# Optimization experiments

Measured on AMD Instinct MI355X. Metric: run time of the kernel, lower is better.

## Reference

```python
import jax, jax.numpy as jnp
import numpy as np


def setup_inputs() -> dict:
    key = jax.random.key(0)
    ks = jax.random.split(key, 5)
    B, S, H, F, E = 2, 2048, 768, 1536, 8
    scale_h = 1.0 / np.sqrt(H)
    scale_f = 1.0 / np.sqrt(F)
    return {
        "hidden_states": jax.random.normal(ks[0], (B, S, H), dtype=jnp.float32),
        "gate_w": jax.random.normal(ks[1], (E, H), dtype=jnp.float32) * scale_h,
        "w1": jax.random.normal(ks[2], (E, F, H), dtype=jnp.float32) * scale_h,
        "w3": jax.random.normal(ks[3], (E, F, H), dtype=jnp.float32) * scale_h,
        "w2": jax.random.normal(ks[4], (E, H, F), dtype=jnp.float32) * scale_f,
        "k": 2,
    }


def reference(hidden_states, gate_w, w1, w3, w2, k):
    B, S, H = hidden_states.shape
    E = gate_w.shape[0]
    x = hidden_states.reshape(-1, H)                     # [T, H]
    T = x.shape[0]

    # Router: softmax in fp32, top-k, renormalize among selected experts.
    router_logits = x @ gate_w.T                         # [T, E]
    probs = jax.nn.softmax(router_logits.astype(jnp.float32), axis=-1)
    top_w, top_i = jax.lax.top_k(probs, k)               # [T, k]
    top_w = top_w / jnp.sum(top_w, axis=-1, keepdims=True)
    top_w = top_w.astype(x.dtype)

    # Scatter top-k weights into dense [T, E] combine weights (0 for unselected).
    combine = jnp.zeros((T, E), dtype=x.dtype)
    combine = combine.at[jnp.arange(T)[:, None], top_i].set(top_w)

    # SwiGLU experts (zero-weight experts contribute exactly 0 to the sum).
    g = jnp.einsum("th,efh->tef", x, w1)                 # [T, E, F]
    u = jnp.einsum("th,efh->tef", x, w3)                 # [T, E, F]
    act = jax.nn.silu(g) * u                             # [T, E, F]
    expert_out = jnp.einsum("tef,ehf->teh", act, w2)     # [T, E, H]
    y = jnp.einsum("te,teh->th", combine, expert_out)    # [T, H]

    return y.reshape(B, S, H), router_logits
```

## Files before the change

kernel.cpp:

```cpp
#include <hip/hip_runtime.h>
#include <hip/hip_bf16.h>

#define T_TOK 4096
#define H_DIM 768
#define E_NUM 8
#define F_DIM 1536

typedef __bf16 bf16x8 __attribute__((ext_vector_type(8)));
typedef unsigned short u16x8 __attribute__((ext_vector_type(8)));
typedef float f32x4 __attribute__((ext_vector_type(4)));
typedef unsigned int u32;

__device__ __forceinline__ unsigned short f2bf(float f) {
    unsigned int u = __float_as_uint(f);
    u += 0x7FFF + ((u >> 16) & 1);
    return (unsigned short)(u >> 16);
}

__device__ __forceinline__ float bf2f(unsigned short s) {
    unsigned int u = ((unsigned int)s) << 16;
    return __uint_as_float(u);
}

__device__ __forceinline__ void gload16(const unsigned short* g, unsigned short* l) {
    __builtin_amdgcn_global_load_lds(
        (const __attribute__((address_space(1))) u32*)(g),
        (__attribute__((address_space(3))) u32*)(l),
        16, 0, 0);
}

__global__ __launch_bounds__(256) void router_kernel(
    const float* __restrict__ x,
    const float* __restrict__ gw,
    float* __restrict__ logits_out,
    float* __restrict__ weight,
    int* __restrict__ eidx,
    unsigned short* __restrict__ xb) {
    int t = blockIdx.x * 4 + (threadIdx.x >> 6);
    int lane = threadIdx.x & 63;

    const float4* xr = reinterpret_cast<const float4*>(x + (size_t)t * H_DIM);
    float4 xv[3];
#pragma unroll
    for (int i = 0; i < 3; ++i) xv[i] = xr[i * 64 + lane];

    unsigned short* xbr = xb + (size_t)t * H_DIM;
#pragma unroll
    for (int i = 0; i < 3; ++i) {
        ushort4 o;
        o.x = f2bf(xv[i].x); o.y = f2bf(xv[i].y);
        o.z = f2bf(xv[i].z); o.w = f2bf(xv[i].w);
        *reinterpret_cast<ushort4*>(xbr + (i * 64 + lane) * 4) = o;
    }

    float v[E_NUM];
#pragma unroll
    for (int e = 0; e < E_NUM; ++e) {
        const float4* g = reinterpret_cast<const float4*>(gw + e * H_DIM);
        float p = 0.f;
#pragma unroll
        for (int i = 0; i < 3; ++i) {
            float4 gv = g[i * 64 + lane];
            p += xv[i].x * gv.x + xv[i].y * gv.y + xv[i].z * gv.z + xv[i].w * gv.w;
        }
        v[e] = p;
    }
#pragma unroll
    for (int d = 1; d < 8; d <<= 1)
#pragma unroll
        for (int e = 0; e < E_NUM; ++e) v[e] += __shfl_xor(v[e], d);
    int me = lane & 7;
    float le = v[0];
#pragma unroll
    for (int e = 1; e < E_NUM; ++e) le = (me == e) ? v[e] : le;
#pragma unroll
    for (int d = 8; d < 64; d <<= 1) le += __shfl_xor(le, d);

    if (lane < 8) logits_out[t * E_NUM + lane] = le;

    float m0 = le;
#pragma unroll
    for (int d = 1; d < 8; d <<= 1) m0 = fmaxf(m0, __shfl_xor(m0, d));
    unsigned long long b0 = __ballot(le == m0);
    int e0 = (__ffsll((long long)b0) - 1) & 7;
    float le1 = (me == e0) ? -3.4e38f : le;
    float m1 = le1;
#pragma unroll
    for (int d = 1; d < 8; d <<= 1) m1 = fmaxf(m1, __shfl_xor(m1, d));
    unsigned long long b1 = __ballot(le1 == m1);
    int e1 = (__ffsll((long long)b1) - 1) & 7;

    if (lane == 0) {
        float w0 = 1.f / (1.f + __expf(m1 - m0));
        weight[t * 2 + 0] = w0;
        weight[t * 2 + 1] = 1.f - w0;
        eidx[t] = e0 | (e1 << 8);
    }
}

__global__ __launch_bounds__(256) void build_lists_kernel(
    const int* __restrict__ eidx,
    int* __restrict__ list,
    int* __restrict__ counts) {
    int e = blockIdx.x;
    int tid = threadIdx.x;
    int lane = tid & 63;
    int wv = tid >> 6;
    __shared__ int wsum[4];
    __shared__ int wbase[4];
    __shared__ int sbase;
    if (tid == 0) sbase = 0;
    __syncthreads();
    for (int c = 0; c < T_TOK; c += 256) {
        int tok = c + tid;
        int pk = eidx[tok];
        int slot = -1;
        if ((pk & 255) == e) slot = tok * 2;
        else if ((pk >> 8) == e) slot = tok * 2 + 1;
        unsigned long long m = __ballot(slot >= 0);
        int prefix = __popcll(m & ((1ull << lane) - 1ull));
        if (lane == 0) wsum[wv] = __popcll(m);
        __syncthreads();
        if (tid == 0) {
            int s = sbase;
#pragma unroll
            for (int i = 0; i < 4; ++i) { wbase[i] = s; s += wsum[i]; }
            sbase = s;
        }
        __syncthreads();
        if (slot >= 0) list[e * T_TOK + wbase[wv] + prefix] = slot;
        __syncthreads();
    }
    if (tid == 0) counts[e] = sbase;
}

__global__ __launch_bounds__(256, 3) void gemm13_kernel(
    const unsigned short* __restrict__ xb,
    const float* __restrict__ w1,
    const float* __restrict__ w3,
    const int* __restrict__ list,
    const int* __restrict__ counts,
    unsigned short* __restrict__ act) {
    int orig = blockIdx.x;
    int wg = (orig & 7) * 768 + (orig >> 3);
    int tm = wg & 31;
    int tn = (wg >> 5) % 24;
    int e = wg / (32 * 24);

    int cnt = counts[e];
    if (tm * 128 >= cnt) return;
    const int* lst = list + e * T_TOK + tm * 128;
    int mrem = cnt - tm * 128;

    __shared__ unsigned short sA[2][128 * 32];
    __shared__ unsigned short sB1[2][64 * 32];
    __shared__ unsigned short sB3[2][64 * 32];

    int tid = threadIdx.x;
    int lane = tid & 63;
    int wid = tid >> 6;

    int r0 = tid >> 2;
    int r1 = r0 + 64;
    int c8 = ((tid & 3) ^ ((r0 >> 1) & 3)) * 8;
    int ldsOff = r0 * 32 + (tid & 3) * 8;
    int tok0 = lst[(r0 < mrem) ? r0 : 0] >> 1;
    int tok1 = lst[(r1 < mrem) ? r1 : 0] >> 1;
    const unsigned short* gA0 = xb + (size_t)tok0 * H_DIM + c8;
    const unsigned short* gA1 = xb + (size_t)tok1 * H_DIM + c8;
    const float* gw1 = w1 + ((size_t)e * F_DIM + tn * 64 + r0) * H_DIM + c8;
    const float* gw3 = w3 + ((size_t)e * F_DIM + tn * 64 + r0) * H_DIM + c8;

    auto writeB = [&](int b, float4 x1a, float4 x1b, float4 x3a, float4 x3b) {
        u16x8 o1, o3;
        o1[0] = f2bf(x1a.x); o1[1] = f2bf(x1a.y); o1[2] = f2bf(x1a.z); o1[3] = f2bf(x1a.w);
        o1[4] = f2bf(x1b.x); o1[5] = f2bf(x1b.y); o1[6] = f2bf(x1b.z); o1[7] = f2bf(x1b.w);
        o3[0] = f2bf(x3a.x); o3[1] = f2bf(x3a.y); o3[2] = f2bf(x3a.z); o3[3] = f2bf(x3a.w);
        o3[4] = f2bf(x3b.x); o3[5] = f2bf(x3b.y); o3[6] = f2bf(x3b.z); o3[7] = f2bf(x3b.w);
        *reinterpret_cast<u16x8*>(&sB1[b][ldsOff]) = o1;
        *reinterpret_cast<u16x8*>(&sB3[b][ldsOff]) = o3;
    };

    int wr = (wid >> 1) * 64;
    int wc = (wid & 1) * 32;
    int fr = lane & 15;
    int kb = ((lane >> 4) ^ ((lane >> 1) & 3)) * 8;

    f32x4 accG[4][2] = {};
    f32x4 accU[4][2] = {};

    const int NT = H_DIM / 32;

    {
        float4 p1a = *reinterpret_cast<const float4*>(gw1);
        float4 p1b = *reinterpret_cast<const float4*>(gw1 + 4);
        float4 p3a = *reinterpret_cast<const float4*>(gw3);
        float4 p3b = *reinterpret_cast<const float4*>(gw3 + 4);
        gload16(gA0, &sA[0][wid * 512]);
        gload16(gA1, &sA[0][2048 + wid * 512]);
        writeB(0, p1a, p1b, p3a, p3b);
    }
    __syncthreads();

    int cur = 0;
    for (int t = 0; t < NT; ++t) {
        float4 n1a, n1b, n3a, n3b;
        bool pre = (t + 1 < NT);
        if (pre) {
            int kt = (t + 1) * 32;
            n1a = *reinterpret_cast<const float4*>(gw1 + kt);
            n1b = *reinterpret_cast<const float4*>(gw1 + kt + 4);
            n3a = *reinterpret_cast<const float4*>(gw3 + kt);
            n3b = *reinterpret_cast<const float4*>(gw3 + kt + 4);
            gload16(gA0 + kt, &sA[cur ^ 1][wid * 512]);
            gload16(gA1 + kt, &sA[cur ^ 1][2048 + wid * 512]);
        }

        bf16x8 a[4], b1[2], b3[2];
#pragma unroll
        for (int mi = 0; mi < 4; ++mi)
            a[mi] = *reinterpret_cast<const bf16x8*>(&sA[cur][(wr + mi * 16 + fr) * 32 + kb]);
#pragma unroll
        for (int ni = 0; ni < 2; ++ni) {
            b1[ni] = *reinterpret_cast<const bf16x8*>(&sB1[cur][(wc + ni * 16 + fr) * 32 + kb]);
            b3[ni] = *reinterpret_cast<const bf16x8*>(&sB3[cur][(wc + ni * 16 + fr) * 32 + kb]);
        }
#pragma unroll
        for (int mi = 0; mi < 4; ++mi)
#pragma unroll
            for (int ni = 0; ni < 2; ++ni) {
                accG[mi][ni] = __builtin_amdgcn_mfma_f32_16x16x32_bf16(a[mi], b1[ni], accG[mi][ni], 0, 0, 0);
                accU[mi][ni] = __builtin_amdgcn_mfma_f32_16x16x32_bf16(a[mi], b3[ni], accU[mi][ni], 0, 0, 0);
            }

        if (pre) writeB(cur ^ 1, n1a, n1b, n3a, n3b);
        __syncthreads();
        cur ^= 1;
    }

    int rg = (lane >> 4) * 4;
    int ci = lane & 15;
#pragma unroll
    for (int mi = 0; mi < 4; ++mi) {
#pragma unroll
        for (int r = 0; r < 4; ++r) {
            int m = wr + mi * 16 + rg + r;
            if (m >= mrem) continue;
            int entry = lst[m];
            size_t rowOff = (size_t)entry * F_DIM + tn * 64;
#pragma unroll
            for (int ni = 0; ni < 2; ++ni) {
                float g = accG[mi][ni][r];
                float u = accU[mi][ni][r];
                float s = g / (1.f + __expf(-g));
                act[rowOff + wc + ni * 16 + ci] = f2bf(s * u);
            }
        }
    }
}

__global__ __launch_bounds__(256, 3) void gemm2_kernel(
    const unsigned short* __restrict__ act,
    const float* __restrict__ w2,
    const int* __restrict__ list,
    const int* __restrict__ counts,
    const float* __restrict__ weight,
    unsigned short* __restrict__ ybuf) {
    int orig = blockIdx.x;
    int wg = (orig & 7) * 192 + (orig >> 3);
    int tm = wg & 31;
    int tn = (wg >> 5) % 6;
    int e = wg / (32 * 6);

    int cnt = counts[e];
    if (tm * 128 >= cnt) return;
    const int* lst = list + e * T_TOK + tm * 128;
    int mrem = cnt - tm * 128;

    __shared__ unsigned short sA[2][128 * 32];
    __shared__ unsigned short sB[2][128 * 32];

    int tid = threadIdx.x;
    int lane = tid & 63;
    int wid = tid >> 6;

    int r0 = tid >> 2;
    int r1 = r0 + 64;
    int c8 = ((tid & 3) ^ ((r0 >> 1) & 3)) * 8;
    int ldsOff = r0 * 32 + (tid & 3) * 8;
    int row0 = lst[(r0 < mrem) ? r0 : 0];
    int row1 = lst[(r1 < mrem) ? r1 : 0];
    const unsigned short* gA0 = act + (size_t)row0 * F_DIM + c8;
    const unsigned short* gA1 = act + (size_t)row1 * F_DIM + c8;
    const float* gw2a = w2 + ((size_t)e * H_DIM + tn * 128 + r0) * F_DIM + c8;
    const float* gw2b = gw2a + (size_t)64 * F_DIM;

    auto writeB = [&](int b, float4 xa0, float4 xa1, float4 xb0, float4 xb1) {
        u16x8 oa, ob;
        oa[0] = f2bf(xa0.x); oa[1] = f2bf(xa0.y); oa[2] = f2bf(xa0.z); oa[3] = f2bf(xa0.w);
        oa[4] = f2bf(xa1.x); oa[5] = f2bf(xa1.y); oa[6] = f2bf(xa1.z); oa[7] = f2bf(xa1.w);
        ob[0] = f2bf(xb0.x); ob[1] = f2bf(xb0.y); ob[2] = f2bf(xb0.z); ob[3] = f2bf(xb0.w);
        ob[4] = f2bf(xb1.x); ob[5] = f2bf(xb1.y); ob[6] = f2bf(xb1.z); ob[7] = f2bf(xb1.w);
        *reinterpret_cast<u16x8*>(&sB[b][ldsOff]) = oa;
        *reinterpret_cast<u16x8*>(&sB[b][2048 + ldsOff]) = ob;
    };

    int wr = (wid >> 1) * 64;
    int wc = (wid & 1) * 64;
    int fr = lane & 15;
    int kb = ((lane >> 4) ^ ((lane >> 1) & 3)) * 8;

    f32x4 acc[4][4] = {};

    const int NT = F_DIM / 32;

    {
        float4 pa0 = *reinterpret_cast<const float4*>(gw2a);
        float4 pa1 = *reinterpret_cast<const float4*>(gw2a + 4);
        float4 pb0 = *reinterpret_cast<const float4*>(gw2b);
        float4 pb1 = *reinterpret_cast<const float4*>(gw2b + 4);
        gload16(gA0, &sA[0][wid * 512]);
        gload16(gA1, &sA[0][2048 + wid * 512]);
        writeB(0, pa0, pa1, pb0, pb1);
    }
    __syncthreads();

    int cur = 0;
    for (int t = 0; t < NT; ++t) {
        float4 na0, na1, nb0, nb1;
        bool pre = (t + 1 < NT);
        if (pre) {
            int kt = (t + 1) * 32;
            na0 = *reinterpret_cast<const float4*>(gw2a + kt);
            na1 = *reinterpret_cast<const float4*>(gw2a + kt + 4);
            nb0 = *reinterpret_cast<const float4*>(gw2b + kt);
            nb1 = *reinterpret_cast<const float4*>(gw2b + kt + 4);
            gload16(gA0 + kt, &sA[cur ^ 1][wid * 512]);
            gload16(gA1 + kt, &sA[cur ^ 1][2048 + wid * 512]);
        }

        bf16x8 a[4], b[4];
#pragma unroll
        for (int mi = 0; mi < 4; ++mi)
            a[mi] = *reinterpret_cast<const bf16x8*>(&sA[cur][(wr + mi * 16 + fr) * 32 + kb]);
#pragma unroll
        for (int ni = 0; ni < 4; ++ni)
            b[ni] = *reinterpret_cast<const bf16x8*>(&sB[cur][(wc + ni * 16 + fr) * 32 + kb]);
#pragma unroll
        for (int mi = 0; mi < 4; ++mi)
#pragma unroll
            for (int ni = 0; ni < 4; ++ni)
                acc[mi][ni] = __builtin_amdgcn_mfma_f32_16x16x32_bf16(a[mi], b[ni], acc[mi][ni], 0, 0, 0);

        if (pre) writeB(cur ^ 1, na0, na1, nb0, nb1);
        __syncthreads();
        cur ^= 1;
    }

    int rg = (lane >> 4) * 4;
    int ci = lane & 15;
#pragma unroll
    for (int mi = 0; mi < 4; ++mi) {
#pragma unroll
        for (int r = 0; r < 4; ++r) {
            int m = wr + mi * 16 + rg + r;
            if (m >= mrem) continue;
            int entry = lst[m];
            float wv = weight[entry];
            size_t rowOff = (size_t)entry * H_DIM + tn * 128;
#pragma unroll
            for (int ni = 0; ni < 4; ++ni)
                ybuf[rowOff + wc + ni * 16 + ci] = f2bf(acc[mi][ni][r] * wv);
        }
    }
}

__global__ __launch_bounds__(256) void combine_kernel(
    const unsigned short* __restrict__ ybuf, float* __restrict__ y) {
    int v = blockIdx.x * blockDim.x + threadIdx.x;
    if (v >= T_TOK * H_DIM / 8) return;
    int t = v / (H_DIM / 8);
    int hv = (v % (H_DIM / 8)) * 8;
    const ushort4* pa = reinterpret_cast<const ushort4*>(ybuf + (size_t)(2 * t) * H_DIM + hv);
    const ushort4* pb = reinterpret_cast<const ushort4*>(ybuf + (size_t)(2 * t + 1) * H_DIM + hv);
    float* yo = y + (size_t)t * H_DIM + hv;
#pragma unroll
    for (int h = 0; h < 2; ++h) {
        ushort4 a = pa[h];
        ushort4 b = pb[h];
        float4 r;
        r.x = bf2f(a.x) + bf2f(b.x);
        r.y = bf2f(a.y) + bf2f(b.y);
        r.z = bf2f(a.z) + bf2f(b.z);
        r.w = bf2f(a.w) + bf2f(b.w);
        *reinterpret_cast<float4*>(yo + h * 4) = r;
    }
}

extern "C" void kernel_launch(void* const* d_in, const int* in_sizes, int n_in,
                              void* d_out, int out_size, void* d_ws, size_t ws_size,
                              hipStream_t stream) {
    const float* x  = (const float*)d_in[0];
    const float* gw = (const float*)d_in[1];
    const float* w1 = (const float*)d_in[2];
    const float* w3 = (const float*)d_in[3];
    const float* w2 = (const float*)d_in[4];

    float* y = (float*)d_out;
    float* logits_out = y + (size_t)T_TOK * H_DIM;

    char* ws = (char*)d_ws;
    size_t off = 0;
    auto alloc = [&](size_t bytes) -> char* {
        char* p = ws + off;
        off += (bytes + 255) & ~(size_t)255;
        return p;
    };
    unsigned short* xb   = (unsigned short*)alloc((size_t)T_TOK * H_DIM * 2);
    unsigned short* act  = (unsigned short*)alloc((size_t)T_TOK * 2 * F_DIM * 2);
    unsigned short* ybuf = (unsigned short*)alloc((size_t)T_TOK * 2 * H_DIM * 2);
    float* weight = (float*)alloc((size_t)T_TOK * 2 * 4);
    int* list     = (int*)alloc((size_t)E_NUM * T_TOK * 4);
    int* counts   = (int*)alloc((size_t)E_NUM * 4);
    int* eidx     = (int*)alloc((size_t)T_TOK * 4);

    router_kernel<<<T_TOK / 4, 256, 0, stream>>>(x, gw, logits_out, weight, eidx, xb);

    build_lists_kernel<<<E_NUM, 256, 0, stream>>>(eidx, list, counts);

    gemm13_kernel<<<6144, 256, 0, stream>>>(xb, w1, w3, list, counts, act);

    gemm2_kernel<<<1536, 256, 0, stream>>>(act, w2, list, counts, weight, ybuf);

    combine_kernel<<<(T_TOK * H_DIM / 8 + 255) / 256, 256, 0, stream>>>(ybuf, y);
}
```

Baseline: 174.1 us.

## Triple-buffer LDS and prefetch two K-tiles ahead in expert GEMMs

Both expert GEMM kernels move from double to triple buffering of the LDS tiles. Global loads for tile t+2 are issued while tile t is computed, with register ping-pong for the fp32 weight prefetch. The __syncthreads is replaced by explicit s_waitcnt vmcnt(6) plus s_barrier, so later loads can stay in flight across the barrier and memory latency is better hidden. The cost is 50% more LDS and more live registers, which could lower occupancy under the 3-waves launch bound, and correctness now depends on the hand-counted vmcnt.

```diff
diff --git a/kernel.cpp b/kernel.cpp
--- a/kernel.cpp
+++ b/kernel.cpp
@@ -10,6 +10,10 @@
 typedef unsigned short u16x8 __attribute__((ext_vector_type(8)));
 typedef float f32x4 __attribute__((ext_vector_type(4)));
 typedef unsigned int u32;
+
+#define WAITV6 asm volatile("s_waitcnt vmcnt(6) lgkmcnt(0)" ::: "memory")
+#define WAITV0 asm volatile("s_waitcnt vmcnt(0) lgkmcnt(0)" ::: "memory")
+#define CFENCE() asm volatile("" ::: "memory")
 
 __device__ __forceinline__ unsigned short f2bf(float f) {
     unsigned int u = __float_as_uint(f);
@@ -152,9 +156,9 @@
     const int* lst = list + e * T_TOK + tm * 128;
     int mrem = cnt - tm * 128;
 
-    __shared__ unsigned short sA[2][128 * 32];
-    __shared__ unsigned short sB1[2][64 * 32];
-    __shared__ unsigned short sB3[2][64 * 32];
+    __shared__ unsigned short sA[3][128 * 32];
+    __shared__ unsigned short sB1[3][64 * 32];
+    __shared__ unsigned short sB3[3][64 * 32];
 
     int tid = threadIdx.x;
     int lane = tid & 63;
@@ -171,12 +175,22 @@
     const float* gw1 = w1 + ((size_t)e * F_DIM + tn * 64 + r0) * H_DIM + c8;
     const float* gw3 = w3 + ((size_t)e * F_DIM + tn * 64 + r0) * H_DIM + c8;
 
-    auto writeB = [&](int b, float4 x1a, float4 x1b, float4 x3a, float4 x3b) {
+    auto stageA = [&](int b, int kt) {
+        gload16(gA0 + kt, &sA[b][wid * 512]);
+        gload16(gA1 + kt, &sA[b][2048 + wid * 512]);
+    };
+    auto loadB = [&](float4 (&p)[4], int kt) {
+        p[0] = *reinterpret_cast<const float4*>(gw1 + kt);
+        p[1] = *reinterpret_cast<const float4*>(gw1 + kt + 4);
+        p[2] = *reinterpret_cast<const float4*>(gw3 + kt);
+        p[3] = *reinterpret_cast<const float4*>(gw3 + kt + 4);
+    };
+    auto writeB = [&](int b, const float4 (&p)[4]) {
         u16x8 o1, o3;
-        o1[0] = f2bf(x1a.x); o1[1] = f2bf(x1a.y); o1[2] = f2bf(x1a.z); o1[3] = f2bf(x1a.w);
-        o1[4] = f2bf(x1b.x); o1[5] = f2bf(x1b.y); o1[6] = f2bf(x1b.z); o1[7] = f2bf(x1b.w);
-        o3[0] = f2bf(x3a.x); o3[1] = f2bf(x3a.y); o3[2] = f2bf(x3a.z); o3[3] = f2bf(x3a.w);
-        o3[4] = f2bf(x3b.x); o3[5] = f2bf(x3b.y); o3[6] = f2bf(x3b.z); o3[7] = f2bf(x3b.w);
+        o1[0] = f2bf(p[0].x); o1[1] = f2bf(p[0].y); o1[2] = f2bf(p[0].z); o1[3] = f2bf(p[0].w);
+        o1[4] = f2bf(p[1].x); o1[5] = f2bf(p[1].y); o1[6] = f2bf(p[1].z); o1[7] = f2bf(p[1].w);
+        o3[0] = f2bf(p[2].x); o3[1] = f2bf(p[2].y); o3[2] = f2bf(p[2].z); o3[3] = f2bf(p[2].w);
+        o3[4] = f2bf(p[3].x); o3[5] = f2bf(p[3].y); o3[6] = f2bf(p[3].z); o3[7] = f2bf(p[3].w);
         *reinterpret_cast<u16x8*>(&sB1[b][ldsOff]) = o1;
         *reinterpret_cast<u16x8*>(&sB3[b][ldsOff]) = o3;
     };
@@ -191,31 +205,19 @@
 
     const int NT = H_DIM / 32;
 
-    {
-        float4 p1a = *reinterpret_cast<const float4*>(gw1);
-        float4 p1b = *reinterpret_cast<const float4*>(gw1 + 4);
-        float4 p3a = *reinterpret_cast<const float4*>(gw3);
-        float4 p3b = *reinterpret_cast<const float4*>(gw3 + 4);
-        gload16(gA0, &sA[0][wid * 512]);
-        gload16(gA1, &sA[0][2048 + wid * 512]);
-        writeB(0, p1a, p1b, p3a, p3b);
-    }
+    float4 pS0[4], pS1[4];
+    stageA(0, 0);  loadB(pS0, 0);
+    stageA(1, 32); loadB(pS1, 32);
+    writeB(0, pS0);
     __syncthreads();
 
-    int cur = 0;
-    for (int t = 0; t < NT; ++t) {
-        float4 n1a, n1b, n3a, n3b;
-        bool pre = (t + 1 < NT);
-        if (pre) {
-            int kt = (t + 1) * 32;
-            n1a = *reinterpret_cast<const float4*>(gw1 + kt);
-            n1b = *reinterpret_cast<const float4*>(gw1 + kt + 4);
-            n3a = *reinterpret_cast<const float4*>(gw3 + kt);
-            n3b = *reinterpret_cast<const float4*>(gw3 + kt + 4);
-            gload16(gA0 + kt, &sA[cur ^ 1][wid * 512]);
-            gload16(gA1 + kt, &sA[cur ^ 1][2048 + wid * 512]);
-        }
-
+    auto doStep = [&](int t, float4 (&ld)[4], float4 (&wr_)[4]) {
+        if (t + 2 < NT) {
+            stageA((t + 2) % 3, (t + 2) * 32);
+            loadB(ld, (t + 2) * 32);
+        }
+        CFENCE();
+        int cur = t % 3;
         bf16x8 a[4], b1[2], b3[2];
 #pragma unroll
         for (int mi = 0; mi < 4; ++mi)
@@ -232,10 +234,18 @@
                 accG[mi][ni] = __builtin_amdgcn_mfma_f32_16x16x32_bf16(a[mi], b1[ni], accG[mi][ni], 0, 0, 0);
                 accU[mi][ni] = __builtin_amdgcn_mfma_f32_16x16x32_bf16(a[mi], b3[ni], accU[mi][ni], 0, 0, 0);
             }
-
-        if (pre) writeB(cur ^ 1, n1a, n1b, n3a, n3b);
-        __syncthreads();
-        cur ^= 1;
+        CFENCE();
+        if (t + 1 < NT) {
+            writeB((t + 1) % 3, wr_);
+            if (t + 2 < NT) { WAITV6; } else { WAITV0; }
+            __builtin_amdgcn_s_barrier();
+            CFENCE();
+        }
+    };
+
+    for (int t = 0; t < NT; t += 2) {
+        doStep(t, pS0, pS1);
+        doStep(t + 1, pS1, pS0);
     }
 
     int rg = (lane >> 4) * 4;
@@ -277,8 +287,8 @@
     const int* lst = list + e * T_TOK + tm * 128;
     int mrem = cnt - tm * 128;
 
-    __shared__ unsigned short sA[2][128 * 32];
-    __shared__ unsigned short sB[2][128 * 32];
+    __shared__ unsigned short sA[3][128 * 32];
+    __shared__ unsigned short sB[3][128 * 32];
 
     int tid = threadIdx.x;
     int lane = tid & 63;
@@ -295,12 +305,22 @@
     const float* gw2a = w2 + ((size_t)e * H_DIM + tn * 128 + r0) * F_DIM + c8;
     const float* gw2b = gw2a + (size_t)64 * F_DIM;
 
-    auto writeB = [&](int b, float4 xa0, float4 xa1, float4 xb0, float4 xb1) {
+    auto stageA = [&](int b, int kt) {
+        gload16(gA0 + kt, &sA[b][wid * 512]);
+        gload16(gA1 + kt, &sA[b][2048 + wid * 512]);
+    };
+    auto loadB = [&](float4 (&p)[4], int kt) {
+        p[0] = *reinterpret_cast<const float4*>(gw2a + kt);
+        p[1] = *reinterpret_cast<const float4*>(gw2a + kt + 4);
+        p[2] = *reinterpret_cast<const float4*>(gw2b + kt);
+        p[3] = *reinterpret_cast<const float4*>(gw2b + kt + 4);
+    };
+    auto writeB = [&](int b, const float4 (&p)[4]) {
         u16x8 oa, ob;
-        oa[0] = f2bf(xa0.x); oa[1] = f2bf(xa0.y); oa[2] = f2bf(xa0.z); oa[3] = f2bf(xa0.w);
-        oa[4] = f2bf(xa1.x); oa[5] = f2bf(xa1.y); oa[6] = f2bf(xa1.z); oa[7] = f2bf(xa1.w);
-        ob[0] = f2bf(xb0.x); ob[1] = f2bf(xb0.y); ob[2] = f2bf(xb0.z); ob[3] = f2bf(xb0.w);
-        ob[4] = f2bf(xb1.x); ob[5] = f2bf(xb1.y); ob[6] = f2bf(xb1.z); ob[7] = f2bf(xb1.w);
+        oa[0] = f2bf(p[0].x); oa[1] = f2bf(p[0].y); oa[2] = f2bf(p[0].z); oa[3] = f2bf(p[0].w);
+        oa[4] = f2bf(p[1].x); oa[5] = f2bf(p[1].y); oa[6] = f2bf(p[1].z); oa[7] = f2bf(p[1].w);
+        ob[0] = f2bf(p[2].x); ob[1] = f2bf(p[2].y); ob[2] = f2bf(p[2].z); ob[3] = f2bf(p[2].w);
+        ob[4] = f2bf(p[3].x); ob[5] = f2bf(p[3].y); ob[6] = f2bf(p[3].z); ob[7] = f2bf(p[3].w);
         *reinterpret_cast<u16x8*>(&sB[b][ldsOff]) = oa;
         *reinterpret_cast<u16x8*>(&sB[b][2048 + ldsOff]) = ob;
     };
@@ -314,31 +334,19 @@
 
     const int NT = F_DIM / 32;
 
-    {
-        float4 pa0 = *reinterpret_cast<const float4*>(gw2a);
-        float4 pa1 = *reinterpret_cast<const float4*>(gw2a + 4);
-        float4 pb0 = *reinterpret_cast<const float4*>(gw2b);
-        float4 pb1 = *reinterpret_cast<const float4*>(gw2b + 4);
-        gload16(gA0, &sA[0][wid * 512]);
-        gload16(gA1, &sA[0][2048 + wid * 512]);
-        writeB(0, pa0, pa1, pb0, pb1);
-    }
+    float4 pS0[4], pS1[4];
+    stageA(0, 0);  loadB(pS0, 0);
+    stageA(1, 32); loadB(pS1, 32);
+    writeB(0, pS0);
     __syncthreads();
 
-    int cur = 0;
-    for (int t = 0; t < NT; ++t) {
-        float4 na0, na1, nb0, nb1;
-        bool pre = (t + 1 < NT);
-        if (pre) {
-            int kt = (t + 1) * 32;
-            na0 = *reinterpret_cast<const float4*>(gw2a + kt);
-            na1 = *reinterpret_cast<const float4*>(gw2a + kt + 4);
-            nb0 = *reinterpret_cast<const float4*>(gw2b + kt);
-            nb1 = *reinterpret_cast<const float4*>(gw2b + kt + 4);
-            gload16(gA0 + kt, &sA[cur ^ 1][wid * 512]);
-            gload16(gA1 + kt, &sA[cur ^ 1][2048 + wid * 512]);
-        }
-
+    auto doStep = [&](int t, float4 (&ld)[4], float4 (&wr_)[4]) {
+        if (t + 2 < NT) {
+            stageA((t + 2) % 3, (t + 2) * 32);
+            loadB(ld, (t + 2) * 32);
+        }
+        CFENCE();
+        int cur = t % 3;
         bf16x8 a[4], b[4];
 #pragma unroll
         for (int mi = 0; mi < 4; ++mi)
@@ -351,10 +359,18 @@
 #pragma unroll
             for (int ni = 0; ni < 4; ++ni)
                 acc[mi][ni] = __builtin_amdgcn_mfma_f32_16x16x32_bf16(a[mi], b[ni], acc[mi][ni], 0, 0, 0);
-
-        if (pre) writeB(cur ^ 1, na0, na1, nb0, nb1);
-        __syncthreads();
-        cur ^= 1;
+        CFENCE();
+        if (t + 1 < NT) {
+            writeB((t + 1) % 3, wr_);
+            if (t + 2 < NT) { WAITV6; } else { WAITV0; }
+            __builtin_amdgcn_s_barrier();
+            CFENCE();
+        }
+    };
+
+    for (int t = 0; t < NT; t += 2) {
+        doStep(t, pS0, pS1);
+        doStep(t + 1, pS1, pS0);
     }
 
     int rg = (lane >> 4) * 4;
```

Measured after the change: 162.8 us. -6.5%, faster.
